# Kernel tuning notes

Measured on AMD Instinct MI355X. Metric: run time of the kernel, lower is better.

## Reference

```python
import jax, jax.numpy as jnp
import numpy as np

T, B, D, H, E = 16, 4096, 256, 512, 32
EPS = 0.1

def setup_inputs() -> dict:
    key = jax.random.key(0)
    ks = jax.random.split(key, 8)
    return {
        "term_emb": jax.random.normal(ks[0], (T, B, D), dtype=jnp.float32),
        "pred_emb": jax.random.normal(ks[1], (E, B, D), dtype=jnp.float32),
        "inv_pred_emb": jax.random.normal(ks[2], (E, B, D), dtype=jnp.float32),
        "signs": jnp.ones((E,), dtype=jnp.float32),
        "W1": jax.random.normal(ks[3], (D, H), dtype=jnp.float32) * (1.0 / np.sqrt(D)),
        "b1": jnp.zeros((H,), dtype=jnp.float32),
        "W2": jax.random.normal(ks[4], (H, D), dtype=jnp.float32) * (1.0 / np.sqrt(H)),
        "b2": jnp.zeros((D,), dtype=jnp.float32),
        "heads": jax.random.randint(ks[5], (E,), 0, T, dtype=jnp.int64),
        "tails": jax.random.randint(ks[6], (E,), 0, T, dtype=jnp.int64),
    }

def reference(term_emb, pred_emb, inv_pred_emb, signs, W1, b1, W2, b2, heads, tails):
    # gather endpoint embeddings per edge: [E, B, D]
    h = term_emb[heads]
    t = term_emb[tails]
    s = signs[:, None, None]
    # estimate_tail_emb (TransE-style NBP): translate by relation embedding
    msg_to_tail = s * (h + pred_emb)      # message along edge direction
    msg_to_head = s * (t + inv_pred_emb)  # message along inverse direction
    # scatter-add messages into per-term slots (sum aggregation)
    agg = (jax.ops.segment_sum(msg_to_tail, tails, num_segments=T)
           + jax.ops.segment_sum(msg_to_head, heads, num_segments=T))
    agg = agg + EPS * term_emb  # residual with eps
    # 1-layer MLP: Linear -> ReLU -> Linear
    hidden = jax.nn.relu(jnp.einsum('tbd,dh->tbh', agg, W1) + b1)
    out = jnp.einsum('tbh,hd->tbd', hidden, W2) + b2
    return out
```

## Files before the change

kernel.cpp:

```cpp
#include <hip/hip_runtime.h>
#include <hip/hip_bf16.h>
#include <stdint.h>

#define T_DIM 16
#define B_DIM 4096
#define D_DIM 256
#define H_DIM 512
#define E_DIM 32
#define M_DIM (T_DIM * B_DIM)
#define BD_DIM (B_DIM * D_DIM)
#define EPS_F 0.1f

#define NSLICE 16
#define SH 32
#define HS_LD 40
#define MAXS 64

typedef __attribute__((ext_vector_type(8))) short short8;
typedef __attribute__((ext_vector_type(4))) float f32x4;

#define GLOBAL_AS __attribute__((address_space(1)))
#define LDS_AS __attribute__((address_space(3)))

__device__ __forceinline__ uint32_t f2bf_rne(float x) {
  uint32_t u = __float_as_uint(x);
  return (u + 0x7fffu + ((u >> 16) & 1u)) >> 16;
}

__global__ __launch_bounds__(256) void agg_prep_kernel(
    const float* __restrict__ term, const float* __restrict__ pred,
    const float* __restrict__ inv, const float* __restrict__ signs,
    const int* __restrict__ heads, const int* __restrict__ tails,
    const float* __restrict__ W1, const float* __restrict__ W2,
    uint16_t* __restrict__ agg, uint16_t* __restrict__ W1T, uint16_t* __restrict__ W2T) {
  const int tid = threadIdx.x;
  if (blockIdx.x >= 1024) {
    const int idx = (blockIdx.x - 1024) * 256 + tid;
    const int d = idx >> 9, h = idx & (H_DIM - 1);
    W1T[h * D_DIM + d] = (uint16_t)f2bf_rne(W1[idx]);
    const int h2 = idx >> 8, d2 = idx & (D_DIM - 1);
    W2T[d2 * H_DIM + h2] = (uint16_t)f2bf_rne(W2[idx]);
    return;
  }

  __shared__ float Cm[T_DIM][T_DIM];
  __shared__ float Lsgn[T_DIM][MAXS];
  __shared__ uint64_t Lptr[T_DIM][MAXS];
  __shared__ int Lcnt[T_DIM];

  Cm[tid >> 4][tid & 15] = ((tid >> 4) == (tid & 15)) ? EPS_F : 0.f;
  if (tid < T_DIM) Lcnt[tid] = 0;
  __syncthreads();
  if (tid < E_DIM) {
    const int e = tid;
    const int hh = heads[e] & (T_DIM - 1);
    const int tt = tails[e] & (T_DIM - 1);
    const float s = signs[e];
    atomicAdd(&Cm[tt][hh], s);
    int i = atomicAdd(&Lcnt[tt], 1);
    Lsgn[tt][i] = s; Lptr[tt][i] = (uint64_t)(pred + (size_t)e * BD_DIM);
    atomicAdd(&Cm[hh][tt], s);
    i = atomicAdd(&Lcnt[hh], 1);
    Lsgn[hh][i] = s; Lptr[hh][i] = (uint64_t)(inv + (size_t)e * BD_DIM);
  }
  __syncthreads();

  const int j = (blockIdx.x * 256 + tid) * 4;

  f32x4 tr[T_DIM];
#pragma unroll
  for (int s = 0; s < T_DIM; ++s)
    tr[s] = __builtin_nontemporal_load(reinterpret_cast<const f32x4*>(term + (size_t)s * BD_DIM + j));

#pragma unroll 2
  for (int t = 0; t < T_DIM; ++t) {
    f32x4 cv[4];
#pragma unroll
    for (int q = 0; q < 4; ++q) cv[q] = *reinterpret_cast<const f32x4*>(&Cm[t][q * 4]);

    float acc[4] = {0.f, 0.f, 0.f, 0.f};
#pragma unroll
    for (int s = 0; s < T_DIM; ++s) {
      const float cs = cv[s >> 2][s & 3];
#pragma unroll
      for (int k = 0; k < 4; ++k) acc[k] += cs * tr[s][k];
    }

    const int n = Lcnt[t];
#pragma unroll 2
    for (int i = 0; i < n; ++i) {
      const float sg = Lsgn[t][i];
      const float* bp = (const float*)Lptr[t][i];
      const f32x4 p = __builtin_nontemporal_load(reinterpret_cast<const f32x4*>(bp + j));
#pragma unroll
      for (int k = 0; k < 4; ++k) acc[k] += sg * p[k];
    }

    uint2 pk;
    pk.x = f2bf_rne(acc[0]) | (f2bf_rne(acc[1]) << 16);
    pk.y = f2bf_rne(acc[2]) | (f2bf_rne(acc[3]) << 16);
    *reinterpret_cast<uint2*>(agg + (size_t)t * BD_DIM + j) = pk;
  }
}

__global__ __launch_bounds__(256, 2) void mlp_fused(
    const uint16_t* __restrict__ A,
    const uint16_t* __restrict__ W1T,
    const uint16_t* __restrict__ W2T,
    const float* __restrict__ b1, const float* __restrict__ b2,
    float* __restrict__ Out) {
  __shared__ __align__(16) uint16_t As[64 * 256];
  __shared__ __align__(16) uint16_t Wb[2][SH * 256];
  __shared__ __align__(16) uint16_t Hs[64 * HS_LD];

  const int tid = threadIdx.x;
  const int w = tid >> 6;
  const int l = tid & 63;
  const int lane16 = l & 15;
  const int quad = l >> 4;
  const int m0 = blockIdx.x * 64;

  const int wm  = (w & 1) * 32;
  const int wnA = ((w >> 1) & 1) * 16;
  const int wn2 = ((w >> 1) & 1) * 128;

#pragma unroll
  for (int p = 0; p < 8; ++p) {
    const int off = p * 2048 + tid * 8;
    const int kc = off >> 11;
    const int row = (off >> 5) & 63;
    const int c = off & 31;
    const uint16_t* g = A + (size_t)(m0 + row) * D_DIM + kc * 32 + c;
    __builtin_amdgcn_global_load_lds((const GLOBAL_AS uint32_t*)g,
                                     (LDS_AS uint32_t*)(As + off), 16, 0, 0);
  }
#pragma unroll
  for (int p = 0; p < 4; ++p) {
    const int off = p * 2048 + tid * 8;
    const int kc = off >> 10;
    const int hl = (off >> 5) & 31;
    const int c = off & 31;
    const uint16_t* g = W1T + (size_t)hl * D_DIM + kc * 32 + c;
    __builtin_amdgcn_global_load_lds((const GLOBAL_AS uint32_t*)g,
                                     (LDS_AS uint32_t*)(Wb[0] + off), 16, 0, 0);
  }
  __syncthreads();

  f32x4 oacc[2][8];
#pragma unroll
  for (int i = 0; i < 2; ++i)
#pragma unroll
    for (int j = 0; j < 8; ++j) oacc[i][j] = (f32x4){0.f, 0.f, 0.f, 0.f};

  for (int s = 0; s < NSLICE; ++s) {
#pragma unroll
    for (int p = 0; p < 4; ++p) {
      const int off = p * 2048 + tid * 8;
      const int d = off >> 5;
      const int c = off & 31;
      const uint16_t* g = W2T + (size_t)d * H_DIM + s * SH + c;
      __builtin_amdgcn_global_load_lds((const GLOBAL_AS uint32_t*)g,
                                       (LDS_AS uint32_t*)(Wb[1] + off), 16, 0, 0);
    }

    f32x4 hacc[2];
#pragma unroll
    for (int i = 0; i < 2; ++i) hacc[i] = (f32x4){0.f, 0.f, 0.f, 0.f};

#pragma unroll
    for (int kk = 0; kk < 8; ++kk) {
      short8 af[2], bfr;
      bfr = *reinterpret_cast<const short8*>(Wb[0] + kk * 1024 + (wnA + lane16) * 32 + quad * 8);
#pragma unroll
      for (int i = 0; i < 2; ++i)
        af[i] = *reinterpret_cast<const short8*>(As + kk * 2048 + (wm + i * 16 + lane16) * 32 + quad * 8);
#pragma unroll
      for (int i = 0; i < 2; ++i)
        hacc[i] = __builtin_amdgcn_mfma_f32_16x16x32_bf16(af[i], bfr, hacc[i], 0, 0, 0);
    }

    {
      const int hloc = wnA + lane16;
      const float bv = b1[s * SH + hloc];
#pragma unroll
      for (int i = 0; i < 2; ++i) {
#pragma unroll
        for (int r = 0; r < 4; ++r) {
          const int row = wm + i * 16 + quad * 4 + r;
          const float x = fmaxf(hacc[i][r] + bv, 0.f);
          Hs[row * HS_LD + hloc] = (uint16_t)f2bf_rne(x);
        }
      }
    }
    __syncthreads();

    if (s < NSLICE - 1) {
#pragma unroll
      for (int p = 0; p < 4; ++p) {
        const int off = p * 2048 + tid * 8;
        const int kc = off >> 10;
        const int hl = (off >> 5) & 31;
        const int c = off & 31;
        const uint16_t* g = W1T + (size_t)((s + 1) * SH + hl) * D_DIM + kc * 32 + c;
        __builtin_amdgcn_global_load_lds((const GLOBAL_AS uint32_t*)g,
                                         (LDS_AS uint32_t*)(Wb[0] + off), 16, 0, 0);
      }
    }

    {
      short8 af2[2], bf2[8];
#pragma unroll
      for (int i = 0; i < 2; ++i)
        af2[i] = *reinterpret_cast<const short8*>(Hs + (wm + i * 16 + lane16) * HS_LD + quad * 8);
#pragma unroll
      for (int j = 0; j < 8; ++j)
        bf2[j] = *reinterpret_cast<const short8*>(Wb[1] + (wn2 + j * 16 + lane16) * 32 + quad * 8);
#pragma unroll
      for (int i = 0; i < 2; ++i)
#pragma unroll
        for (int j = 0; j < 8; ++j)
          oacc[i][j] = __builtin_amdgcn_mfma_f32_16x16x32_bf16(af2[i], bf2[j], oacc[i][j], 0, 0, 0);
    }
    __syncthreads();
  }

#pragma unroll
  for (int j = 0; j < 8; ++j) {
    const int col = wn2 + j * 16 + lane16;
    const float bv = b2[col];
#pragma unroll
    for (int i = 0; i < 2; ++i) {
#pragma unroll
      for (int r = 0; r < 4; ++r) {
        const int row = m0 + wm + i * 16 + quad * 4 + r;
        Out[(size_t)row * D_DIM + col] = oacc[i][j][r] + bv;
      }
    }
  }
}

extern "C" void kernel_launch(void* const* d_in, const int* in_sizes, int n_in,
                              void* d_out, int out_size, void* d_ws, size_t ws_size,
                              hipStream_t stream) {
  const float* term  = (const float*)d_in[0];
  const float* pred  = (const float*)d_in[1];
  const float* inv   = (const float*)d_in[2];
  const float* signs = (const float*)d_in[3];
  const float* W1    = (const float*)d_in[4];
  const float* b1    = (const float*)d_in[5];
  const float* W2    = (const float*)d_in[6];
  const float* b2    = (const float*)d_in[7];
  const int* heads   = (const int*)d_in[8];
  const int* tails   = (const int*)d_in[9];

  char* ws = (char*)d_ws;
  uint16_t* W1T = (uint16_t*)(ws);
  uint16_t* W2T = (uint16_t*)(ws + 262144);
  uint16_t* agg = (uint16_t*)(ws + 524288);

  agg_prep_kernel<<<dim3(1536), dim3(256), 0, stream>>>(
      term, pred, inv, signs, heads, tails, W1, W2, agg, W1T, W2T);
  mlp_fused<<<dim3(M_DIM / 64), dim3(256), 0, stream>>>(
      agg, W1T, W2T, b1, b2, (float*)d_out);
}
```

Baseline: 392.4 us.

## Load MLP weight fragments directly into registers and double-buffer hidden tile

The fused MLP kernel stops staging W1 and W2 slices through shared memory. Each wave now loads its MFMA B-operand fragments straight from global memory (L2-resident) into registers, with the next W1 slice prefetched during the second GEMM. The hidden tile buffer is double-buffered so the trailing barrier per slice can be dropped. This cuts LDS traffic, LDS footprint and one barrier per iteration, at the cost of more VGPRs and per-wave global loads that are less coalesced and exposed to latency.

```diff
diff --git a/kernel.cpp b/kernel.cpp
--- a/kernel.cpp
+++ b/kernel.cpp
@@ -110,8 +110,7 @@
     const float* __restrict__ b1, const float* __restrict__ b2,
     float* __restrict__ Out) {
   __shared__ __align__(16) uint16_t As[64 * 256];
-  __shared__ __align__(16) uint16_t Wb[2][SH * 256];
-  __shared__ __align__(16) uint16_t Hs[64 * HS_LD];
+  __shared__ __align__(16) uint16_t Hs[2][64 * HS_LD];
 
   const int tid = threadIdx.x;
   const int w = tid >> 6;
@@ -134,16 +133,13 @@
     __builtin_amdgcn_global_load_lds((const GLOBAL_AS uint32_t*)g,
                                      (LDS_AS uint32_t*)(As + off), 16, 0, 0);
   }
-#pragma unroll
-  for (int p = 0; p < 4; ++p) {
-    const int off = p * 2048 + tid * 8;
-    const int kc = off >> 10;
-    const int hl = (off >> 5) & 31;
-    const int c = off & 31;
-    const uint16_t* g = W1T + (size_t)hl * D_DIM + kc * 32 + c;
-    __builtin_amdgcn_global_load_lds((const GLOBAL_AS uint32_t*)g,
-                                     (LDS_AS uint32_t*)(Wb[0] + off), 16, 0, 0);
-  }
+
+  short8 w1f[8];
+#pragma unroll
+  for (int kk = 0; kk < 8; ++kk)
+    w1f[kk] = *reinterpret_cast<const short8*>(
+        W1T + (size_t)(wnA + lane16) * D_DIM + kk * 32 + quad * 8);
+
   __syncthreads();
 
   f32x4 oacc[2][8];
@@ -153,42 +149,37 @@
     for (int j = 0; j < 8; ++j) oacc[i][j] = (f32x4){0.f, 0.f, 0.f, 0.f};
 
   for (int s = 0; s < NSLICE; ++s) {
-#pragma unroll
-    for (int p = 0; p < 4; ++p) {
-      const int off = p * 2048 + tid * 8;
-      const int d = off >> 5;
-      const int c = off & 31;
-      const uint16_t* g = W2T + (size_t)d * H_DIM + s * SH + c;
-      __builtin_amdgcn_global_load_lds((const GLOBAL_AS uint32_t*)g,
-                                       (LDS_AS uint32_t*)(Wb[1] + off), 16, 0, 0);
-    }
+    short8 w2f[8];
+#pragma unroll
+    for (int j = 0; j < 8; ++j)
+      w2f[j] = *reinterpret_cast<const short8*>(
+          W2T + (size_t)(wn2 + j * 16 + lane16) * H_DIM + s * SH + quad * 8);
 
     f32x4 hacc[2];
 #pragma unroll
     for (int i = 0; i < 2; ++i) hacc[i] = (f32x4){0.f, 0.f, 0.f, 0.f};
-
 #pragma unroll
     for (int kk = 0; kk < 8; ++kk) {
-      short8 af[2], bfr;
-      bfr = *reinterpret_cast<const short8*>(Wb[0] + kk * 1024 + (wnA + lane16) * 32 + quad * 8);
+      short8 af[2];
 #pragma unroll
       for (int i = 0; i < 2; ++i)
         af[i] = *reinterpret_cast<const short8*>(As + kk * 2048 + (wm + i * 16 + lane16) * 32 + quad * 8);
 #pragma unroll
       for (int i = 0; i < 2; ++i)
-        hacc[i] = __builtin_amdgcn_mfma_f32_16x16x32_bf16(af[i], bfr, hacc[i], 0, 0, 0);
+        hacc[i] = __builtin_amdgcn_mfma_f32_16x16x32_bf16(af[i], w1f[kk], hacc[i], 0, 0, 0);
     }
 
     {
       const int hloc = wnA + lane16;
       const float bv = b1[s * SH + hloc];
+      uint16_t* hsb = Hs[s & 1];
 #pragma unroll
       for (int i = 0; i < 2; ++i) {
 #pragma unroll
         for (int r = 0; r < 4; ++r) {
           const int row = wm + i * 16 + quad * 4 + r;
           const float x = fmaxf(hacc[i][r] + bv, 0.f);
-          Hs[row * HS_LD + hloc] = (uint16_t)f2bf_rne(x);
+          hsb[row * HS_LD + hloc] = (uint16_t)f2bf_rne(x);
         }
       }
     }
@@ -196,32 +187,23 @@
 
     if (s < NSLICE - 1) {
 #pragma unroll
-      for (int p = 0; p < 4; ++p) {
-        const int off = p * 2048 + tid * 8;
-        const int kc = off >> 10;
-        const int hl = (off >> 5) & 31;
-        const int c = off & 31;
-        const uint16_t* g = W1T + (size_t)((s + 1) * SH + hl) * D_DIM + kc * 32 + c;
-        __builtin_amdgcn_global_load_lds((const GLOBAL_AS uint32_t*)g,
-                                         (LDS_AS uint32_t*)(Wb[0] + off), 16, 0, 0);
-      }
+      for (int kk = 0; kk < 8; ++kk)
+        w1f[kk] = *reinterpret_cast<const short8*>(
+            W1T + (size_t)((s + 1) * SH + wnA + lane16) * D_DIM + kk * 32 + quad * 8);
     }
 
     {
-      short8 af2[2], bf2[8];
-#pragma unroll
-      for (int i = 0; i < 2; ++i)
-        af2[i] = *reinterpret_cast<const short8*>(Hs + (wm + i * 16 + lane16) * HS_LD + quad * 8);
-#pragma unroll
-      for (int j = 0; j < 8; ++j)
-        bf2[j] = *reinterpret_cast<const short8*>(Wb[1] + (wn2 + j * 16 + lane16) * 32 + quad * 8);
+      const uint16_t* hsb = Hs[s & 1];
+      short8 af2[2];
+#pragma unroll
+      for (int i = 0; i < 2; ++i)
+        af2[i] = *reinterpret_cast<const short8*>(hsb + (wm + i * 16 + lane16) * HS_LD + quad * 8);
 #pragma unroll
       for (int i = 0; i < 2; ++i)
 #pragma unroll
         for (int j = 0; j < 8; ++j)
-          oacc[i][j] = __builtin_amdgcn_mfma_f32_16x16x32_bf16(af2[i], bf2[j], oacc[i][j], 0, 0, 0);
-    }
-    __syncthreads();
+          oacc[i][j] = __builtin_amdgcn_mfma_f32_16x16x32_bf16(af2[i], w2f[j], oacc[i][j], 0, 0, 0);
+    }
   }
 
 #pragma unroll
```

Result: slower. 448.8 us (+14.4%).
